# Kernel optimization log

Hardware: AMD Instinct MI355X
Metric: run time of the kernel (lower is better)

The kernel has to match this reference:

```python
import jax, jax.numpy as jnp
import numpy as np

D = 2048
NH = 16
DH = D // NH          # 128
DC = D // 4           # 512  (KV latent)
DCQ = D // 2          # 1024 (Q latent)
B = 1
L = 2048
MAX_LEN = 4096


def precompute_rope(dh, max_len):
    inv_freq = 1.0 / (10000.0 ** (jnp.arange(0, dh, 2, dtype=jnp.float32) / dh))
    t = jnp.arange(max_len, dtype=jnp.float32)
    freqs = jnp.outer(t, inv_freq)                 # [max_len, dh/2]
    emb = jnp.concatenate([freqs, freqs], axis=-1) # [max_len, dh]
    return jnp.cos(emb), jnp.sin(emb)


def apply_rope(t, cos, sin):
    # t: [B, H, L, dh]; cos/sin: [L, dh]
    x1, x2 = jnp.split(t, 2, axis=-1)
    rot = jnp.concatenate([-x2, x1], axis=-1)
    return t * cos + rot * sin


def setup_inputs() -> dict:
    key = jax.random.key(0)
    ks = jax.random.split(key, 9)
    s = 0.02
    return {
        "x": jax.random.normal(ks[0], (B, L, D), dtype=jnp.float32),
        "W_DKV": jax.random.normal(ks[1], (D, DC), dtype=jnp.float32) * s,
        "W_UK": jax.random.normal(ks[2], (DC, NH * DH), dtype=jnp.float32) * s,
        "W_UV": jax.random.normal(ks[3], (DC, NH * DH), dtype=jnp.float32) * s,
        "W_DQ": jax.random.normal(ks[4], (D, DCQ), dtype=jnp.float32) * s,
        "W_UQ": jax.random.normal(ks[5], (DCQ, 2 * NH * DH), dtype=jnp.float32) * s,
        "W_lam": jax.random.normal(ks[6], (D, NH), dtype=jnp.float32) * s,
        "b_lam": jnp.zeros((NH,), dtype=jnp.float32),
        "W_out": jax.random.normal(ks[7], (D, D), dtype=jnp.float32) * s,
    }


def reference(x, W_DKV, W_UK, W_UV, W_DQ, W_UQ, W_lam, b_lam, W_out):
    Bx, Lx, Dx = x.shape
    cos, sin = precompute_rope(DH, MAX_LEN)
    cos, sin = cos[:Lx], sin[:Lx]

    # MLA KV compression: single K/V shared by the paired query heads
    c_kv = x @ W_DKV                                            # [B, L, dc]
    k = (c_kv @ W_UK).reshape(Bx, Lx, NH, DH).transpose(0, 2, 1, 3)   # [B, nh, L, dh]
    v = (c_kv @ W_UV).reshape(Bx, Lx, NH, DH).transpose(0, 2, 1, 3)   # [B, nh, L, dh]

    # Low-rank Q, doubled heads for differential attention
    c_q = x @ W_DQ                                              # [B, L, dcq]
    q = (c_q @ W_UQ).reshape(Bx, Lx, 2 * NH, DH).transpose(0, 2, 1, 3)  # [B, 2nh, L, dh]

    q = apply_rope(q, cos, sin)
    k = apply_rope(k, cos, sin)

    # Group paired heads (2i, 2i+1) share k/v head i -> avoid repeat_interleave
    qp = q.reshape(Bx, NH, 2, Lx, DH)                           # [B, nh, 2, L, dh]
    scale = 1.0 / jnp.sqrt(jnp.asarray(DH, dtype=x.dtype))
    scores = jnp.einsum('bhpqd,bhkd->bhpqk', qp, k) * scale     # [B, nh, 2, L, L]
    causal = jnp.tril(jnp.ones((Lx, Lx), dtype=bool))
    scores = jnp.where(causal, scores, jnp.asarray(-jnp.inf, dtype=scores.dtype))
    probs = jax.nn.softmax(scores, axis=-1)
    attn = jnp.einsum('bhpqk,bhkd->bhpqd', probs, v)            # [B, nh, 2, L, dh]
    attn1, attn2 = attn[:, :, 0], attn[:, :, 1]                 # [B, nh, L, dh]

    # Token-specific sigmoid lambda per head
    lam = jax.nn.sigmoid(x @ W_lam + b_lam)                     # [B, L, nh]
    lam = lam.transpose(0, 2, 1)[..., None]                     # [B, nh, L, 1]

    out = (attn1 - lam * attn2).transpose(0, 2, 1, 3).reshape(Bx, Lx, Dx)
    return out @ W_out
```

## Files before the change

kernel.cpp:

```cpp
#include <hip/hip_runtime.h>
#include <cstdint>
#include <cstddef>

typedef __bf16 bf16x8 __attribute__((ext_vector_type(8)));
typedef __bf16 bf16x4 __attribute__((ext_vector_type(4)));
typedef float f32x4 __attribute__((ext_vector_type(4)));


template <int N> __device__ __forceinline__ void waitcnt_vm() {
  if constexpr (N == 2)      asm volatile("s_waitcnt vmcnt(2)" ::: "memory");
  else if constexpr (N == 3) asm volatile("s_waitcnt vmcnt(3)" ::: "memory");
  else if constexpr (N == 4) asm volatile("s_waitcnt vmcnt(4)" ::: "memory");
  else if constexpr (N == 6) asm volatile("s_waitcnt vmcnt(6)" ::: "memory");
  else if constexpr (N == 8) asm volatile("s_waitcnt vmcnt(8)" ::: "memory");
  else                       asm volatile("s_waitcnt vmcnt(0)" ::: "memory");
}

template <int BM, int NKS, int NW>
__device__ __forceinline__ void gemm_core(const __bf16* __restrict__ A,
                                          const __bf16* __restrict__ Bt,
                                          int K, int bm, int bn,
                                          __bf16* As, __bf16* Bs,
                                          f32x4 (*acc)[128 / ((NW / 2) * 16)]) {
  const int tid = threadIdx.x;
  const int w = tid >> 6;
  const int lane = tid & 63;
  const int quad = lane >> 4;
  const int l16 = lane & 15;
  constexpr int WM = (BM == 128) ? 64 : 32;
  constexpr int WN = 128 / (NW / 2);
  constexpr int MI = WM / 16;
  constexpr int NJ = WN / 16;
  const int wm = (w & 1) * WM;
  const int wn = (w >> 1) * WN;
  const int srow = lane >> 2;
  const int sseg = (lane & 3) * 8;

  auto stage = [&](int k0, int buf) {
#pragma unroll
    for (int ks = 0; ks < NKS; ++ks) {
#pragma unroll
      for (int g = w; g < BM / 16; g += NW) {
        const __bf16* ga = A + (size_t)(bm + g * 16 + srow) * K + k0 + ks * 32 + sseg;
        __builtin_amdgcn_global_load_lds(
            (const __attribute__((address_space(1))) void*)ga,
            (__attribute__((address_space(3))) void*)&As[(buf * NKS + ks) * (BM * 32) + g * 512],
            16, 0, 0);
      }
#pragma unroll
      for (int g = w; g < 8; g += NW) {
        const __bf16* gb = Bt + (size_t)(bn + g * 16 + srow) * K + k0 + ks * 32 + sseg;
        __builtin_amdgcn_global_load_lds(
            (const __attribute__((address_space(1))) void*)gb,
            (__attribute__((address_space(3))) void*)&Bs[(buf * NKS + ks) * 4096 + g * 512],
            16, 0, 0);
      }
    }
  };

#pragma unroll
  for (int i = 0; i < MI; ++i)
#pragma unroll
    for (int j = 0; j < NJ; ++j) acc[i][j] = (f32x4){0.f, 0.f, 0.f, 0.f};

  asm volatile("s_waitcnt vmcnt(0)" ::: "memory");
  stage(0, 0);

  const int NIT = K / (32 * NKS);
  for (int it = 0; it < NIT; ++it) {
    const int cur = it & 1;
    if (it + 1 < NIT) {
      stage((it + 1) * 32 * NKS, cur ^ 1);
      if constexpr (NW == 4) {
        waitcnt_vm<NKS * (BM / 64 + 2)>();
      } else {
        if (w < BM / 16) waitcnt_vm<NKS * 2>();
        else             waitcnt_vm<NKS * 1>();
      }
    } else {
      waitcnt_vm<0>();
    }
    __builtin_amdgcn_s_barrier();
    asm volatile("" ::: "memory");
    const __bf16* Ab = &As[cur * NKS * (BM * 32)];
    const __bf16* Bb = &Bs[cur * NKS * 4096];
#pragma unroll
    for (int ks = 0; ks < NKS; ++ks) {
      bf16x8 af[MI], bfr[NJ];
#pragma unroll
      for (int i = 0; i < MI; ++i)
        af[i] = *(const bf16x8*)&Ab[ks * (BM * 32) + (wm + i * 16 + l16) * 32 + quad * 8];
#pragma unroll
      for (int j = 0; j < NJ; ++j)
        bfr[j] = *(const bf16x8*)&Bb[ks * 4096 + (wn + j * 16 + l16) * 32 + quad * 8];
#pragma unroll
      for (int i = 0; i < MI; ++i)
#pragma unroll
        for (int j = 0; j < NJ; ++j)
          acc[i][j] = __builtin_amdgcn_mfma_f32_16x16x32_bf16(af[i], bfr[j],
                                                              acc[i][j], 0, 0, 0);
    }
    asm volatile("s_waitcnt lgkmcnt(0)" ::: "memory");
    __builtin_amdgcn_s_barrier();
    asm volatile("" ::: "memory");
  }
}

template <int BM, int NKS, bool BF16OUT, int NW = 4>
__device__ __forceinline__ void gemm_body(const __bf16* __restrict__ A,
                                          const __bf16* __restrict__ Bt,
                                          void* __restrict__ Cv,
                                          int N, int K, int bm, int bn,
                                          __bf16* As, __bf16* Bs) {
  constexpr int WM = (BM == 128) ? 64 : 32;
  constexpr int WN = 128 / (NW / 2);
  constexpr int MI = WM / 16;
  constexpr int NJ = WN / 16;
  f32x4 acc[MI][NJ];
  gemm_core<BM, NKS, NW>(A, Bt, K, bm, bn, As, Bs, acc);
  const int tid = threadIdx.x;
  const int w = tid >> 6, lane = tid & 63, quad = lane >> 4, l16 = lane & 15;
  const int wm = (w & 1) * WM, wn = (w >> 1) * WN;
#pragma unroll
  for (int i = 0; i < MI; ++i)
#pragma unroll
    for (int j = 0; j < NJ; ++j)
#pragma unroll
      for (int r = 0; r < 4; ++r) {
        const int row = bm + wm + i * 16 + quad * 4 + r;
        const int col = bn + wn + j * 16 + l16;
        if constexpr (BF16OUT)
          ((__bf16*)Cv)[(size_t)row * N + col] = (__bf16)acc[i][j][r];
        else
          ((float*)Cv)[(size_t)row * N + col] = acc[i][j][r];
      }
}

template <int BM, int NKS, bool BF16OUT, int NW = 4>
__global__ __launch_bounds__(NW * 64) void gemm_mfma(const __bf16* __restrict__ A,
                                                     const __bf16* __restrict__ Bt,
                                                     void* __restrict__ Cv,
                                                     int M, int N, int K) {
  __shared__ __bf16 As[2 * BM * 32 * NKS];
  __shared__ __bf16 Bs[2 * 128 * 32 * NKS];
  gemm_body<BM, NKS, BF16OUT, NW>(A, Bt, Cv, N, K, blockIdx.y * BM, blockIdx.x * 128, As, Bs);
}

__device__ __forceinline__ void transpose_tile(const float* __restrict__ src,
                                               __bf16* __restrict__ dst,
                                               int K, int N, int kx, int ny,
                                               float (*T)[36], int st) {
  const int k0 = kx * 32;
  const int n0 = ny * 32;
  const int r = st >> 3;
  const int c = (st & 7) * 4;
  *(float4*)&T[r][c] = *(const float4*)&src[(size_t)(k0 + r) * N + n0 + c];
  __syncthreads();
  bf16x4 o = {(__bf16)T[c + 0][r], (__bf16)T[c + 1][r],
              (__bf16)T[c + 2][r], (__bf16)T[c + 3][r]};
  *(bf16x4*)&dst[(size_t)(n0 + r) * K + k0 + c] = o;
}

__global__ __launch_bounds__(512) void down_lam(
    const __bf16* __restrict__ x_bf, const __bf16* __restrict__ WtDKV,
    const __bf16* __restrict__ WtDQ, __bf16* __restrict__ c_kv,
    __bf16* __restrict__ c_q, const __bf16* __restrict__ WlT,
    const float* __restrict__ b_lam, float* __restrict__ lam,
    const float* __restrict__ W_UK, const float* __restrict__ W_UV,
    const float* __restrict__ W_UQ, __bf16* __restrict__ tUK,
    __bf16* __restrict__ tUV, __bf16* __restrict__ tUQ,
    float* __restrict__ cosT, float* __restrict__ sinT) {
  __shared__ __bf16 As[2 * 64 * 32 * 2];
  __shared__ __bf16 Bs[2 * 128 * 32 * 2];
  int id = blockIdx.x;
  const int tid = threadIdx.x;
  if (id < 416) {
    const int bxl = id >> 5, by = id & 31;
    if (bxl == 12) {
      if (by >= 16) return;
      const int w = tid >> 6, lane = tid & 63, quad = lane >> 4, l16 = lane & 15;
      const int m0 = (by * 8 + w) * 16;
      const __bf16* xrow = x_bf + (size_t)(m0 + l16) * 2048 + quad * 8;
      const __bf16* wrow = WlT + (size_t)l16 * 2048 + quad * 8;
      f32x4 acc[4];
#pragma unroll
      for (int u = 0; u < 4; ++u) acc[u] = (f32x4){0.f, 0.f, 0.f, 0.f};
      for (int k0 = 0; k0 < 2048; k0 += 128) {
#pragma unroll
        for (int u = 0; u < 4; ++u) {
          bf16x8 a = *(const bf16x8*)&xrow[k0 + u * 32];
          bf16x8 b = *(const bf16x8*)&wrow[k0 + u * 32];
          acc[u] = __builtin_amdgcn_mfma_f32_16x16x32_bf16(a, b, acc[u], 0, 0, 0);
        }
      }
      const float bl = b_lam[l16];
#pragma unroll
      for (int r = 0; r < 4; ++r) {
        const float v = acc[0][r] + acc[1][r] + acc[2][r] + acc[3][r] + bl;
        lam[(size_t)(m0 + quad * 4 + r) * 16 + l16] = 1.0f / (1.0f + __expf(-v));
      }
      return;
    }
    if (bxl < 4)
      gemm_body<64, 2, true, 8>(x_bf, WtDKV, (void*)c_kv, 512, 2048,
                                by * 64, bxl * 128, As, Bs);
    else
      gemm_body<64, 2, true, 8>(x_bf, WtDQ, (void*)c_q, 1024, 2048,
                                by * 64, (bxl - 4) * 128, As, Bs);
    return;
  }
  id -= 416;
  if (id < 3072) {
    int t = id * 2 + (tid >> 8);
    const int st = tid & 255;
    float (*T)[36] = (float(*)[36])((char*)As + (tid >> 8) * 4608);
    if (t < 1024)
      transpose_tile(W_UK, tUK, 512, 2048, t & 15, t >> 4, T, st);
    else if (t < 2048) {
      t -= 1024;
      transpose_tile(W_UV, tUV, 512, 2048, t & 15, t >> 4, T, st);
    } else {
      t -= 2048;
      transpose_tile(W_UQ, tUQ, 1024, 4096, t & 31, t >> 5, T, st);
    }
    return;
  }
  id -= 3072;
  {
    const int l = id * 4 + (tid >> 7);
    const int d = tid & 127;
    const int j = d & 63;
    const float inv = exp2f(-(float)j * 0.2076205059304601f);
    const float ang = (float)l * inv;
    cosT[l * 128 + d] = cosf(ang);
    sinT[l * 128 + d] = sinf(ang);
  }
}

__global__ __launch_bounds__(256) void up_fused3(
    const __bf16* __restrict__ c_kv, const __bf16* __restrict__ WtUK,
    const __bf16* __restrict__ WtUV, const __bf16* __restrict__ c_q,
    const __bf16* __restrict__ WtUQ, __bf16* __restrict__ k_bf,
    __bf16* __restrict__ v_t, __bf16* __restrict__ q_bf,
    const float* __restrict__ cosT, const float* __restrict__ sinT) {
  __shared__ __align__(16) char usm[32768];
  __bf16* As = (__bf16*)usm;
  __bf16* Bs = (__bf16*)(usm + 16384);
  const int bx = blockIdx.x;
  const int bm = blockIdx.y * 128;
  const int tid = threadIdx.x;
  const int w = tid >> 6, lane = tid & 63, quad = lane >> 4, l16 = lane & 15;
  const int wm = (w & 1) * 64, wn = (w >> 1) * 64;
  f32x4 acc[4][4];
  if (bx < 16) {
    const int bn = bx * 128;
    gemm_core<128, 1, 4>(c_kv, WtUK, 512, bm, bn, As, Bs, acc);
    __bf16 (*Kt)[128] = (__bf16(*)[128])usm;
#pragma unroll
    for (int i = 0; i < 4; ++i)
#pragma unroll
      for (int j = 0; j < 4; ++j)
#pragma unroll
        for (int r = 0; r < 4; ++r)
          Kt[wm + i * 16 + quad * 4 + r][wn + j * 16 + l16] = (__bf16)acc[i][j][r];
    __syncthreads();
#pragma unroll
    for (int j = 0; j < 4; ++j) {
      const int d = wn + j * 16 + l16;
      const float sgn = (d < 64) ? -1.f : 1.f;
#pragma unroll
      for (int i = 0; i < 4; ++i)
#pragma unroll
        for (int r = 0; r < 4; ++r) {
          const int lr = wm + i * 16 + quad * 4 + r;
          const int l = bm + lr;
          const float v = (float)Kt[lr][d];
          const float pr = (float)Kt[lr][d ^ 64];
          const float ov = v * cosT[l * 128 + d] + sgn * pr * sinT[l * 128 + d];
          k_bf[(size_t)l * 2048 + bn + d] = (__bf16)ov;
        }
    }
  } else if (bx < 32) {
    const int bn = (bx - 16) * 128;
    gemm_core<128, 1, 4>(c_kv, WtUV, 512, bm, bn, As, Bs, acc);
#pragma unroll
    for (int i = 0; i < 4; ++i)
#pragma unroll
      for (int j = 0; j < 4; ++j) {
        const int d = bn + wn + j * 16 + l16;
        const int l = bm + wm + i * 16 + quad * 4;
        bf16x4 pk = {(__bf16)acc[i][j][0], (__bf16)acc[i][j][1],
                     (__bf16)acc[i][j][2], (__bf16)acc[i][j][3]};
        *(bf16x4*)&v_t[(size_t)d * 2048 + l] = pk;
      }
  } else {
    const int bn = (bx - 32) * 128;
    gemm_core<128, 1, 4>(c_q, WtUQ, 1024, bm, bn, As, Bs, acc);
#pragma unroll
    for (int i = 0; i < 4; ++i)
#pragma unroll
      for (int j = 0; j < 4; ++j)
#pragma unroll
        for (int r = 0; r < 4; ++r) {
          const int row = bm + wm + i * 16 + quad * 4 + r;
          const int col = bn + wn + j * 16 + l16;
          q_bf[(size_t)row * 4096 + col] = (__bf16)acc[i][j][r];
        }
  }
}

__global__ __launch_bounds__(256) void prep_all(
    const float* __restrict__ W_DKV, const float* __restrict__ W_DQ,
    const float* __restrict__ x,     const float* __restrict__ W_lam,
    __bf16* __restrict__ tDKV, __bf16* __restrict__ tDQ,
    __bf16* __restrict__ x_bf, __bf16* __restrict__ WlT) {
  __shared__ float T[32][36];
  int t = blockIdx.x;
  const int tid = threadIdx.x;
  if (t < 3072) {
    if (t < 1024)
      transpose_tile(W_DKV, tDKV, 2048, 512, t & 63, t >> 6, T, tid);
    else {
      t -= 1024;
      transpose_tile(W_DQ, tDQ, 2048, 1024, t & 63, t >> 6, T, tid);
    }
    return;
  }
  t -= 3072;
  if (t < 4096) {
    const int i = t * 256 + tid;
    float4 v = *(const float4*)&x[(size_t)i * 4];
    bf16x4 o = {(__bf16)v.x, (__bf16)v.y, (__bf16)v.z, (__bf16)v.w};
    *(bf16x4*)&x_bf[(size_t)i * 4] = o;
    return;
  }
  t -= 4096;
  {
    const int i = t * 256 + tid;
    const int k = i >> 4, n = i & 15;
    WlT[(size_t)n * 2048 + k] = (__bf16)W_lam[i];
  }
}

__global__ __launch_bounds__(512, 2) void attn_kernel3(
    const __bf16* __restrict__ Qb, const __bf16* __restrict__ Kb,
    const __bf16* __restrict__ Vt, const float* __restrict__ cosT,
    const float* __restrict__ sinT, const float* __restrict__ lam,
    __bf16* __restrict__ y, const float* __restrict__ W_out,
    __bf16* __restrict__ Wt_out) {
  __shared__ __align__(16) char smem[81920];
  float (*Ex)[132] = (float(*)[132])smem;

  const int bx = blockIdx.x;
  const int tid = threadIdx.x;
  if (bx >= 512) {
    const int t = (bx - 512) * 2 + (tid >> 8);
    const int st = tid & 255;
    float (*T)[36] = (float(*)[36])(smem + (tid >> 8) * 4608);
    const int k0 = (t & 63) * 32;
    const int n0 = (t >> 6) * 32;
    const int r = st >> 3;
    const int c = (st & 7) * 4;
    *(float4*)&T[r][c] = *(const float4*)&W_out[(size_t)(k0 + r) * 2048 + n0 + c];
    __syncthreads();
    bf16x4 o = {(__bf16)T[c + 0][r], (__bf16)T[c + 1][r],
                (__bf16)T[c + 2][r], (__bf16)T[c + 3][r]};
    *(bf16x4*)&Wt_out[(size_t)(n0 + r) * 2048 + k0 + c] = o;
    return;
  }
  const int hv = bx >> 8;
  const int ii = bx & 255;
  const int qt = hv ? (ii >> 4) : 31 - (ii >> 4);
  const int hk = ii & 15;
  const int q0 = qt * 64;
  const int w = tid >> 6, lane = tid & 63, quad = lane >> 4, l16 = lane & 15;
  const int wrow = (w & 3) * 16;
  const int qoff = (2 * hk + (w >> 2)) * 128;
  const int kvoff = hk * 128;
  const float qscale = 0.08838834764831845f;
  char* Pw = smem + 65536 + w * 2048;

  bf16x8 aq[4];
  {
    const int l = q0 + wrow + l16;
    const size_t qbase = (size_t)l * 4096 + qoff + quad * 8;
    bf16x8 raw[4];
#pragma unroll
    for (int ks = 0; ks < 4; ++ks)
      raw[ks] = *(const bf16x8*)&Qb[qbase + ks * 32];
#pragma unroll
    for (int ks = 0; ks < 4; ++ks) {
      const float* cp = &cosT[l * 128 + ks * 32 + quad * 8];
      const float* sp = &sinT[l * 128 + ks * 32 + quad * 8];
#pragma unroll
      for (int j = 0; j < 8; ++j) {
        const float cv = cp[j];
        const float sv = sp[j];
        const float rot = (ks < 2) ? -(float)raw[ks + 2][j] : (float)raw[ks - 2][j];
        aq[ks][j] = (__bf16)(((float)raw[ks][j] * cv + rot * sv) * qscale);
      }
    }
  }

  auto stage = [&](int kt_, char* buf) {
    const int k0_ = kt_ * 64;
    __bf16* Ksb = (__bf16*)buf;
    __bf16* Vsb = (__bf16*)(buf + 16384);
#pragma unroll
    for (int d = 0; d < 2; ++d) {
      const int r0 = w * 8 + d * 4;
      const int row = r0 + (lane >> 4);
      const int ck = (lane & 15) ^ (row & 15);
      const __bf16* ga = Kb + (size_t)(k0_ + row) * 2048 + kvoff + ck * 8;
      __builtin_amdgcn_global_load_lds(
          (const __attribute__((address_space(1))) void*)ga,
          (__attribute__((address_space(3))) void*)&Ksb[r0 * 128], 16, 0, 0);
      const int r0v = w * 16 + d * 8;
      const int rowv = r0v + (lane >> 3);
      const int cv = (lane & 7) ^ (rowv & 7);
      const __bf16* gv = Vt + (size_t)(kvoff + rowv) * 2048 + k0_ + cv * 8;
      __builtin_amdgcn_global_load_lds(
          (const __attribute__((address_space(1))) void*)gv,
          (__attribute__((address_space(3))) void*)&Vsb[r0v * 64], 16, 0, 0);
    }
  };

  f32x4 o[8];
#pragma unroll
  for (int i = 0; i < 8; ++i) o[i] = (f32x4){0.f, 0.f, 0.f, 0.f};
  float m = -1e30f, lsum = 0.f;

  asm volatile("s_waitcnt vmcnt(0)" ::: "memory");
  stage(0, smem);

  for (int kt = 0; kt <= qt; ++kt) {
    const int cur = kt & 1;
    __bf16* Ks = (__bf16*)(smem + cur * 32768);
    __bf16* Vs = (__bf16*)(smem + cur * 32768 + 16384);
    const int k0 = kt * 64;
    if (kt < qt) {
      stage(kt + 1, smem + (cur ^ 1) * 32768);
      asm volatile("s_waitcnt vmcnt(4)" ::: "memory");
    } else {
      asm volatile("s_waitcnt vmcnt(0)" ::: "memory");
    }
    __builtin_amdgcn_s_barrier();
    asm volatile("" ::: "memory");
    f32x4 st[4];
#pragma unroll
    for (int t = 0; t < 4; ++t) st[t] = (f32x4){0.f, 0.f, 0.f, 0.f};
    __builtin_amdgcn_s_setprio(1);
#pragma unroll
    for (int ks = 0; ks < 4; ++ks) {
#pragma unroll
      for (int t = 0; t < 4; ++t) {
        bf16x8 ak = *(bf16x8*)&Ks[(t * 16 + l16) * 128 + (((ks * 4 + quad) ^ l16) << 3)];
        st[t] = __builtin_amdgcn_mfma_f32_16x16x32_bf16(ak, aq[ks], st[t], 0, 0, 0);
      }
    }
    __builtin_amdgcn_s_setprio(0);
    {
      const int q = q0 + wrow + l16;
      float rm = -1e30f;
      if (kt != qt) {
#pragma unroll
        for (int t = 0; t < 4; ++t)
#pragma unroll
          for (int r = 0; r < 4; ++r) rm = fmaxf(rm, st[t][r]);
      } else {
#pragma unroll
        for (int t = 0; t < 4; ++t)
#pragma unroll
          for (int r = 0; r < 4; ++r) {
            const int key = k0 + t * 16 + quad * 4 + r;
            if (key > q) st[t][r] = -1e30f;
            rm = fmaxf(rm, st[t][r]);
          }
      }
      rm = fmaxf(rm, __shfl_xor(rm, 16, 64));
      rm = fmaxf(rm, __shfl_xor(rm, 32, 64));
      const float mn = fmaxf(m, rm);
      float rs = 0.f;
#pragma unroll
      for (int t = 0; t < 4; ++t)
#pragma unroll
        for (int r = 0; r < 4; ++r) {
          st[t][r] = __expf(st[t][r] - mn);
          rs += st[t][r];
        }
      rs += __shfl_xor(rs, 16, 64);
      rs += __shfl_xor(rs, 32, 64);
      if (__any(rm > m)) {
        const float alpha = __expf(m - mn);
        lsum = lsum * alpha + rs;
        m = mn;
#pragma unroll
        for (int r = 0; r < 4; ++r) {
          const float ar = __shfl(alpha, quad * 4 + r, 64);
#pragma unroll
          for (int nt = 0; nt < 8; ++nt) o[nt][r] *= ar;
        }
      } else {
        lsum += rs;
      }
      const int prow = l16;
#pragma unroll
      for (int t = 0; t < 4; ++t) {
        bf16x4 pk = {(__bf16)st[t][0], (__bf16)st[t][1],
                     (__bf16)st[t][2], (__bf16)st[t][3]};
        const int wch = (t * 2 + (quad >> 1)) ^ (prow & 7);
        *(bf16x4*)(Pw + prow * 128 + wch * 16 + (quad & 1) * 8) = pk;
      }
    }
    __builtin_amdgcn_s_setprio(1);
#pragma unroll
    for (int ks = 0; ks < 2; ++ks) {
      const int rch = ((ks * 4 + quad) ^ (l16 & 7)) << 4;
      bf16x8 pa = *(bf16x8*)(Pw + l16 * 128 + rch);
#pragma unroll
      for (int nt = 0; nt < 8; ++nt) {
        bf16x8 bv = *(bf16x8*)&Vs[(nt * 16 + l16) * 64 + (((ks * 4 + quad) ^ (l16 & 7)) << 3)];
        o[nt] = __builtin_amdgcn_mfma_f32_16x16x32_bf16(pa, bv, o[nt], 0, 0, 0);
      }
    }
    __builtin_amdgcn_s_setprio(0);
    asm volatile("s_waitcnt lgkmcnt(0)" ::: "memory");
    __builtin_amdgcn_s_barrier();
    asm volatile("" ::: "memory");
  }
  const float linv = 1.0f / lsum;
  if (w >= 4) {
#pragma unroll
    for (int r = 0; r < 4; ++r) {
      const float inv = __shfl(linv, quad * 4 + r, 64);
      const int rr = wrow + quad * 4 + r;
#pragma unroll
      for (int nt = 0; nt < 8; ++nt)
        Ex[rr][nt * 16 + l16] = o[nt][r] * inv;
    }
  }
  __syncthreads();
  if (w < 4) {
#pragma unroll
    for (int r = 0; r < 4; ++r) {
      const float inv = __shfl(linv, quad * 4 + r, 64);
      const int rr = wrow + quad * 4 + r;
      const int l = q0 + rr;
      const float lm = lam[l * 16 + hk];
      __bf16* dst = y + (size_t)l * 2048 + hk * 128;
#pragma unroll
      for (int nt = 0; nt < 8; ++nt) {
        const float v1 = o[nt][r] * inv;
        dst[nt * 16 + l16] = (__bf16)(v1 - lm * Ex[rr][nt * 16 + l16]);
      }
    }
  }
}

extern "C" void kernel_launch(void* const* d_in, const int* in_sizes, int n_in,
                              void* d_out, int out_size, void* d_ws, size_t ws_size,
                              hipStream_t stream) {
  const float* x     = (const float*)d_in[0];
  const float* W_DKV = (const float*)d_in[1];
  const float* W_UK  = (const float*)d_in[2];
  const float* W_UV  = (const float*)d_in[3];
  const float* W_DQ  = (const float*)d_in[4];
  const float* W_UQ  = (const float*)d_in[5];
  const float* W_lam = (const float*)d_in[6];
  const float* b_lam = (const float*)d_in[7];
  const float* W_out = (const float*)d_in[8];
  float* out = (float*)d_out;

  char* ws = (char*)d_ws;
  #define MB(n) ((size_t)(n) << 20)
  __bf16* x_bf   = (__bf16*)(ws + MB(0));
  __bf16* Wt_DKV = (__bf16*)(ws + MB(8));
  __bf16* Wt_DQ  = (__bf16*)(ws + MB(10));
  __bf16* c_kv   = (__bf16*)(ws + MB(14));
  __bf16* c_q    = (__bf16*)(ws + MB(16));
  __bf16* Wt_UK  = (__bf16*)(ws + MB(20));
  __bf16* Wt_UV  = (__bf16*)(ws + MB(22));
  __bf16* Wt_UQ  = (__bf16*)(ws + MB(24));
  __bf16* k_bf   = (__bf16*)(ws + MB(32));
  __bf16* y_bf   = (__bf16*)(ws + MB(40));
  __bf16* q_bf   = (__bf16*)(ws + MB(48));
  __bf16* v_t    = (__bf16*)(ws + MB(64));
  float*  lam    = (float*)(ws + MB(88));
  float*  cosT   = (float*)(ws + MB(89));
  float*  sinT   = (float*)(ws + MB(90));
  __bf16* WlT    = (__bf16*)(ws + MB(91));
  __bf16* Wt_out = (__bf16*)(ws + MB(92));

  prep_all<<<7296, 256, 0, stream>>>(W_DKV, W_DQ, x, W_lam,
                                     Wt_DKV, Wt_DQ, x_bf, WlT);
  down_lam<<<4000, 512, 0, stream>>>(x_bf, Wt_DKV, Wt_DQ, c_kv, c_q,
                                     WlT, b_lam, lam,
                                     W_UK, W_UV, W_UQ, Wt_UK, Wt_UV, Wt_UQ,
                                     cosT, sinT);
  up_fused3<<<dim3(64, 16), 256, 0, stream>>>(c_kv, Wt_UK, Wt_UV, c_q, Wt_UQ,
                                              k_bf, v_t, q_bf, cosT, sinT);
  attn_kernel3<<<2560, 512, 0, stream>>>(q_bf, k_bf, v_t, cosT, sinT, lam,
                                         y_bf, W_out, Wt_out);
  gemm_mfma<64, 2, false, 8><<<dim3(16, 32), 512, 0, stream>>>(y_bf, Wt_out, out, 2048, 2048, 2048);
}
```

Before: 278.5 us.

## Shrink attention query tile to 32 rows with 256-thread blocks

Attention blocks now cover 32 query rows with 4 waves (two per paired head) instead of 64 rows with 8 waves, giving twice as many blocks and interleaving heavy and light causal tiles. K/V staging drops double buffering to a single 40 KB shared buffer, so more blocks can be resident per CU. The W_out transpose tail now calls a shared transpose_tile helper. In exchange, each K/V tile is loaded twice as often, and load latency is no longer hidden by prefetching within a block.

```diff
diff --git a/kernel.cpp b/kernel.cpp
--- a/kernel.cpp
+++ b/kernel.cpp
@@ -342,43 +342,39 @@
   }
 }
 
-__global__ __launch_bounds__(512, 2) void attn_kernel3(
+__global__ __launch_bounds__(256, 4) void attn_kernel5(
     const __bf16* __restrict__ Qb, const __bf16* __restrict__ Kb,
     const __bf16* __restrict__ Vt, const float* __restrict__ cosT,
     const float* __restrict__ sinT, const float* __restrict__ lam,
     __bf16* __restrict__ y, const float* __restrict__ W_out,
     __bf16* __restrict__ Wt_out) {
-  __shared__ __align__(16) char smem[81920];
-  float (*Ex)[132] = (float(*)[132])smem;
+  __shared__ __align__(16) char smem[40960];
 
   const int bx = blockIdx.x;
   const int tid = threadIdx.x;
-  if (bx >= 512) {
-    const int t = (bx - 512) * 2 + (tid >> 8);
-    const int st = tid & 255;
-    float (*T)[36] = (float(*)[36])(smem + (tid >> 8) * 4608);
-    const int k0 = (t & 63) * 32;
-    const int n0 = (t >> 6) * 32;
-    const int r = st >> 3;
-    const int c = (st & 7) * 4;
-    *(float4*)&T[r][c] = *(const float4*)&W_out[(size_t)(k0 + r) * 2048 + n0 + c];
-    __syncthreads();
-    bf16x4 o = {(__bf16)T[c + 0][r], (__bf16)T[c + 1][r],
-                (__bf16)T[c + 2][r], (__bf16)T[c + 3][r]};
-    *(bf16x4*)&Wt_out[(size_t)(n0 + r) * 2048 + k0 + c] = o;
+  if (bx >= 1024) {
+    const int t = bx - 1024;
+    float (*T)[36] = (float(*)[36])smem;
+    transpose_tile(W_out, Wt_out, 2048, 2048, t & 63, t >> 6, T, tid);
     return;
   }
-  const int hv = bx >> 8;
-  const int ii = bx & 255;
-  const int qt = hv ? (ii >> 4) : 31 - (ii >> 4);
-  const int hk = ii & 15;
-  const int q0 = qt * 64;
+  const int kk = bx >> 8;
+  const int cc = bx & 255;
+  const int g = cc >> 4;
+  const int hk = cc & 15;
+  const int qt = (kk == 0) ? 63 - g : (kk == 1) ? g
+               : (kk == 2) ? 47 - g : 16 + g;
+  const int q0 = qt * 32;
+  const int NT = (qt >> 1) + 1;
   const int w = tid >> 6, lane = tid & 63, quad = lane >> 4, l16 = lane & 15;
-  const int wrow = (w & 3) * 16;
-  const int qoff = (2 * hk + (w >> 2)) * 128;
+  const int wrow = (w & 1) * 16;
+  const int qoff = (2 * hk + (w >> 1)) * 128;
   const int kvoff = hk * 128;
   const float qscale = 0.08838834764831845f;
-  char* Pw = smem + 65536 + w * 2048;
+  __bf16* Ks = (__bf16*)smem;
+  __bf16* Vs = (__bf16*)(smem + 16384);
+  char* Pw = smem + 32768 + w * 2048;
+  float (*Ex)[128] = (float(*)[128])smem;
 
   bf16x8 aq[4];
   {
@@ -402,26 +398,24 @@
     }
   }
 
-  auto stage = [&](int kt_, char* buf) {
+  auto stage = [&](int kt_) {
     const int k0_ = kt_ * 64;
-    __bf16* Ksb = (__bf16*)buf;
-    __bf16* Vsb = (__bf16*)(buf + 16384);
-#pragma unroll
-    for (int d = 0; d < 2; ++d) {
-      const int r0 = w * 8 + d * 4;
+#pragma unroll
+    for (int d = 0; d < 4; ++d) {
+      const int r0 = w * 16 + d * 4;
       const int row = r0 + (lane >> 4);
       const int ck = (lane & 15) ^ (row & 15);
       const __bf16* ga = Kb + (size_t)(k0_ + row) * 2048 + kvoff + ck * 8;
       __builtin_amdgcn_global_load_lds(
           (const __attribute__((address_space(1))) void*)ga,
-          (__attribute__((address_space(3))) void*)&Ksb[r0 * 128], 16, 0, 0);
-      const int r0v = w * 16 + d * 8;
+          (__attribute__((address_space(3))) void*)&Ks[r0 * 128], 16, 0, 0);
+      const int r0v = w * 32 + d * 8;
       const int rowv = r0v + (lane >> 3);
       const int cv = (lane & 7) ^ (rowv & 7);
       const __bf16* gv = Vt + (size_t)(kvoff + rowv) * 2048 + k0_ + cv * 8;
       __builtin_amdgcn_global_load_lds(
           (const __attribute__((address_space(1))) void*)gv,
-          (__attribute__((address_space(3))) void*)&Vsb[r0v * 64], 16, 0, 0);
+          (__attribute__((address_space(3))) void*)&Vs[r0v * 64], 16, 0, 0);
     }
   };
 
@@ -431,19 +425,11 @@
   float m = -1e30f, lsum = 0.f;
 
   asm volatile("s_waitcnt vmcnt(0)" ::: "memory");
-  stage(0, smem);
-
-  for (int kt = 0; kt <= qt; ++kt) {
-    const int cur = kt & 1;
-    __bf16* Ks = (__bf16*)(smem + cur * 32768);
-    __bf16* Vs = (__bf16*)(smem + cur * 32768 + 16384);
+
+  for (int kt = 0; kt < NT; ++kt) {
     const int k0 = kt * 64;
-    if (kt < qt) {
-      stage(kt + 1, smem + (cur ^ 1) * 32768);
-      asm volatile("s_waitcnt vmcnt(4)" ::: "memory");
-    } else {
-      asm volatile("s_waitcnt vmcnt(0)" ::: "memory");
-    }
+    stage(kt);
+    asm volatile("s_waitcnt vmcnt(0)" ::: "memory");
     __builtin_amdgcn_s_barrier();
     asm volatile("" ::: "memory");
     f32x4 st[4];
@@ -462,7 +448,7 @@
     {
       const int q = q0 + wrow + l16;
       float rm = -1e30f;
-      if (kt != qt) {
+      if (kt != NT - 1) {
 #pragma unroll
         for (int t = 0; t < 4; ++t)
 #pragma unroll
@@ -529,7 +515,7 @@
     asm volatile("" ::: "memory");
   }
   const float linv = 1.0f / lsum;
-  if (w >= 4) {
+  if (w >= 2) {
 #pragma unroll
     for (int r = 0; r < 4; ++r) {
       const float inv = __shfl(linv, quad * 4 + r, 64);
@@ -540,7 +526,7 @@
     }
   }
   __syncthreads();
-  if (w < 4) {
+  if (w < 2) {
 #pragma unroll
     for (int r = 0; r < 4; ++r) {
       const float inv = __shfl(linv, quad * 4 + r, 64);
@@ -599,7 +585,7 @@
                                      cosT, sinT);
   up_fused3<<<dim3(64, 16), 256, 0, stream>>>(c_kv, Wt_UK, Wt_UV, c_q, Wt_UQ,
                                               k_bf, v_t, q_bf, cosT, sinT);
-  attn_kernel3<<<2560, 512, 0, stream>>>(q_bf, k_bf, v_t, cosT, sinT, lam,
+  attn_kernel5<<<5120, 256, 0, stream>>>(q_bf, k_bf, v_t, cosT, sinT, lam,
                                          y_bf, W_out, Wt_out);
   gemm_mfma<64, 2, false, 8><<<dim3(16, 32), 512, 0, stream>>>(y_bf, Wt_out, out, 2048, 2048, 2048);
 }
```

Result: slower. 288.6 us (+3.6%).
